# Optimization experiments

Hardware: AMD Instinct MI355X
Metric: run time of the kernel (lower is better)

## Reference

```python
import jax, jax.numpy as jnp
import numpy as np

B, T, IN, HID, HYP = 32, 1024, 512, 512, 256


def setup_inputs() -> dict:
    key = jax.random.key(0)
    ks = jax.random.split(key, 12)
    s = lambda *sh: 1.0 / np.sqrt(sh[-1])
    return {
        "x": jax.random.normal(ks[0], (B, T, IN), jnp.float32),
        "hidden": jax.random.normal(ks[1], (B, HID), jnp.float32),
        "W_start": jax.random.uniform(ks[2], (HYP, IN), jnp.float32, -s(HYP, IN), s(HYP, IN)),
        "b_start": jax.random.uniform(ks[3], (HYP,), jnp.float32, -s(HYP, IN), s(HYP, IN)),
        "W_mid": jax.random.uniform(ks[4], (HYP, HYP), jnp.float32, -s(HYP, HYP), s(HYP, HYP)),
        "b_mid": jax.random.uniform(ks[5], (HYP,), jnp.float32, -s(HYP, HYP), s(HYP, HYP)),
        "W_end": jax.random.uniform(ks[6], (HID, HYP), jnp.float32, -s(HID, HYP), s(HID, HYP)),
        "b_end": jax.random.uniform(ks[7], (HID,), jnp.float32, -s(HID, HYP), s(HID, HYP)),
        "W2": jax.random.uniform(ks[8], (HID, IN), jnp.float32, -s(HID, IN), s(HID, IN)),
        "b2": jax.random.uniform(ks[9], (HID,), jnp.float32, -s(HID, IN), s(HID, IN)),
    }


def _roll_sum_relu(b, hidden):
    # b: [B, T, H], hidden: [B, H]
    # recurrence: h_t = relu(roll(h_{t-1}, 1, axis=-1) + b_t)
    bt = jnp.swapaxes(b, 0, 1)  # [T, B, H]

    def step(h, b_t):
        h_new = jax.nn.relu(jnp.roll(h, 1, axis=-1) + b_t)
        return h_new, h_new

    _, outs = jax.lax.scan(step, hidden, bt)
    return jnp.swapaxes(outs, 0, 1)  # [B, T, H]


def reference(x, hidden, W_start, b_start, W_mid, b_mid, W_end, b_end, W2, b2):
    h = jax.nn.relu(jnp.einsum('bti,hi->bth', x, W_start) + b_start)
    h = jax.nn.relu(jnp.einsum('bth,gh->btg', h, W_mid) + b_mid)
    fc_end = jnp.einsum('btg,og->bto', h, W_end) + b_end
    sig = jax.nn.sigmoid(jnp.einsum('bti,oi->bto', x, W2) + b2)
    b = fc_end * sig  # [B, T, HID]
    outputs = _roll_sum_relu(b, hidden)
    return outputs, outputs[:, -1, :]
```

## Files before the change

### kernel.cpp

```cpp
#include <hip/hip_runtime.h>
#include <math.h>

#define B_   32
#define T_   1024
#define IN_  512
#define HID_ 512
#define HYP_ 256
#define M_   (B_ * T_)
#define R_   128
#define NSEG 8
#define SEGL 128
#define NCH  (B_ * HID_)

#define H1S  0
#define H2S  65536
#define STG  131072
#define LDS_BYTES 163840

typedef _Float16 half8_t __attribute__((ext_vector_type(8)));
typedef float    f32x4   __attribute__((ext_vector_type(4)));

typedef __attribute__((address_space(1))) const void* gptr_as1;
typedef __attribute__((address_space(3))) void*       lptr_as3;

__device__ __forceinline__ void gload_lds16(const void* g, void* l) {
    __builtin_amdgcn_global_load_lds((gptr_as1)g, (lptr_as3)l, 16, 0, 0);
}

#define VMCNT8() asm volatile("s_waitcnt vmcnt(8)" ::: "memory")
#define VMCNT4() asm volatile("s_waitcnt vmcnt(4)" ::: "memory")
#define VMCNT0() asm volatile("s_waitcnt vmcnt(0)" ::: "memory")
#define LGKM0()  asm volatile("s_waitcnt lgkmcnt(0)" ::: "memory")
#define SBAR()   __builtin_amdgcn_s_barrier()
#define SCHED0() __builtin_amdgcn_sched_barrier(0)

__global__ __launch_bounds__(256) void cvt_w(
    const float* __restrict__ Ws, _Float16* __restrict__ wsh,
    const float* __restrict__ Wm, _Float16* __restrict__ wmh,
    const float* __restrict__ We, _Float16* __restrict__ weh,
    const float* __restrict__ W2, _Float16* __restrict__ w2h)
{
    const int blk = blockIdx.x;
    const float* src; _Float16* dst; int base;
    if      (blk < 64)  { src = Ws; dst = wsh; base = blk; }
    else if (blk < 96)  { src = Wm; dst = wmh; base = blk - 64; }
    else if (blk < 160) { src = We; dst = weh; base = blk - 96; }
    else                { src = W2; dst = w2h; base = blk - 160; }
    const int i = base * 2048 + threadIdx.x * 8;
    f32x4 v0 = *(const f32x4*)(src + i);
    f32x4 v1 = *(const f32x4*)(src + i + 4);
    half8_t h;
    h[0] = (_Float16)v0[0]; h[1] = (_Float16)v0[1];
    h[2] = (_Float16)v0[2]; h[3] = (_Float16)v0[3];
    h[4] = (_Float16)v1[0]; h[5] = (_Float16)v1[1];
    h[6] = (_Float16)v1[2]; h[7] = (_Float16)v1[3];
    *(half8_t*)(dst + i) = h;
}

__device__ __forceinline__ void stage512(const _Float16* src, int K,
                                         char* ldsbase, int tid)
{
#pragma unroll
    for (int q = 0; q < 2; ++q) {
        const int s = q * 512 + tid;
        const int g = s >> 6, c2 = (s >> 4) & 3, r = (s & 15) ^ c2;
        const char* gp = (const char*)src + (size_t)(g * 16 + r) * (K * 2) + c2 * 16;
        char* lp = ldsbase + (q * 512 + (tid & ~63)) * 16;
        gload_lds16(gp, lp);
    }
}

__device__ __forceinline__ void stageW64(const _Float16* src, int K,
                                         char* ldsbase, int tid)
{
    stage512(src,      K, ldsbase,         tid);
    stage512(src + 32, K, ldsbase + 16384, tid);
}

__device__ __forceinline__ void ld_x32(const float* __restrict__ x, int m0,
                                       int ks, int tid, f32x4& a, f32x4& b)
{
    const int g = tid >> 6, c2 = (tid >> 4) & 3, r = (tid & 15) ^ c2;
    const float* p = x + (size_t)(m0 + g * 16 + r) * IN_ + ks + c2 * 8;
    a = *(const f32x4*)p;
    b = *(const f32x4*)(p + 4);
}

__device__ __forceinline__ void wr_x32(const f32x4& a, const f32x4& b,
                                       char* ldsbase, int tid)
{
    half8_t h;
    h[0] = (_Float16)a[0]; h[1] = (_Float16)a[1];
    h[2] = (_Float16)a[2]; h[3] = (_Float16)a[3];
    h[4] = (_Float16)b[0]; h[5] = (_Float16)b[1];
    h[6] = (_Float16)b[2]; h[7] = (_Float16)b[3];
    *(half8_t*)(ldsbase + tid * 16) = h;
}

__device__ __forceinline__ void do_step16(const char* ab, const char* bb,
                                          int wm, int wn, int lsw,
                                          f32x4 acc[4][4])
{
    half8_t af[4], wf[4];
#pragma unroll
    for (int i = 0; i < 4; ++i)
        af[i] = *(const half8_t*)(ab + (wm * 4 + i) * 1024 + lsw);
#pragma unroll
    for (int j = 0; j < 4; ++j)
        wf[j] = *(const half8_t*)(bb + (wn * 4 + j) * 1024 + lsw);
#pragma unroll
    for (int i = 0; i < 4; ++i)
#pragma unroll
        for (int j = 0; j < 4; ++j)
            acc[i][j] = __builtin_amdgcn_mfma_f32_16x16x32_f16(af[i], wf[j], acc[i][j], 0, 0, 0);
}

__device__ __forceinline__ void do_step32(const char* ab, const char* bb,
                                          int wm, int wn, int lsw,
                                          f32x4 acc[4][4])
{
    do_step16(ab,        bb,         wm, wn, lsw, acc);
    do_step16(ab + 8192, bb + 16384, wm, wn, lsw, acc);
}

__device__ __forceinline__ void epi_relu_lds(char* dst, const f32x4 acc[4][4],
                                             const float* __restrict__ bias,
                                             int wm, int wn, int lq, int lr)
{
#pragma unroll
    for (int j = 0; j < 4; ++j) {
        const int col = wn * 64 + j * 16 + lr;
        const float bv = bias[col];
        const int cc2 = (col & 31) >> 3;
        const int cpart = (col >> 5) * 8192 + cc2 * 256 + (col & 7) * 2;
#pragma unroll
        for (int i = 0; i < 4; ++i) {
#pragma unroll
            for (int rg = 0; rg < 4; ++rg) {
                const int row = wm * 64 + i * 16 + lq * 4 + rg;
                const float v = fmaxf(acc[i][j][rg] + bv, 0.f);
                *(_Float16*)(dst + cpart + (row >> 4) * 1024 +
                             (((row & 15) ^ cc2)) * 16) = (_Float16)v;
            }
        }
    }
}

__global__ __launch_bounds__(512, 2) void fused_mlp(
    const float* __restrict__ x,
    const _Float16* __restrict__ wsh, const float* __restrict__ bs,
    const _Float16* __restrict__ wmh, const float* __restrict__ bm,
    const _Float16* __restrict__ weh, const float* __restrict__ be,
    const _Float16* __restrict__ w2h, const float* __restrict__ b2,
    _Float16* __restrict__ bh)
{
    __shared__ __align__(16) char lds[LDS_BYTES];

    const int tid  = threadIdx.x;
    const int m0   = blockIdx.x * R_;
    const int lane = tid & 63;
    const int wave = tid >> 6;
    const int wm = wave >> 2;
    const int wn = wave & 3;
    const int lq = lane >> 4, lr = lane & 15;
    const int lsw = (lane ^ ((lane >> 4) & 3)) * 16;

    const f32x4 zero = {0.f, 0.f, 0.f, 0.f};

    {
        f32x4 acc[4][4];
#pragma unroll
        for (int i = 0; i < 4; ++i)
#pragma unroll
            for (int j = 0; j < 4; ++j) acc[i][j] = zero;

        {
            f32x4 pa0, pa1, pa2, pa3;
            ld_x32(x, m0, 0, tid, pa0, pa1);
            ld_x32(x, m0, 32, tid, pa2, pa3);
            stageW64(wsh, IN_, lds + STG, tid);
            wr_x32(pa0, pa1, lds + H2S, tid);
            wr_x32(pa2, pa3, lds + H2S + 8192, tid);
            __syncthreads();
        }
        for (int s = 0; s < 7; ++s) {
            const int e = s + 1;
            f32x4 pa0, pa1, pa2, pa3;
            ld_x32(x, m0, e * 64, tid, pa0, pa1);
            ld_x32(x, m0, e * 64 + 32, tid, pa2, pa3);
            SCHED0();
            stageW64(wsh + e * 64, IN_, (e & 1) ? lds + H2S + 32768 : lds + STG, tid);
            SCHED0(); VMCNT8(); SCHED0(); SBAR(); SCHED0();
            char* xb = lds + H2S + (e & 1) * 16384;
            wr_x32(pa0, pa1, xb, tid);
            wr_x32(pa2, pa3, xb + 8192, tid);
            const char* ab = lds + H2S + (s & 1) * 16384;
            const char* bb = (s & 1) ? lds + H2S + 32768 : lds + STG;
            __builtin_amdgcn_s_setprio(1);
            do_step32(ab, bb, wm, wn, lsw, acc);
            __builtin_amdgcn_s_setprio(0);
            LGKM0(); SCHED0(); SBAR(); SCHED0();
        }
        stageW64(wmh, HYP_, lds + STG, tid);
        SCHED0(); VMCNT4(); SCHED0(); SBAR(); SCHED0();
        __builtin_amdgcn_s_setprio(1);
        do_step32(lds + H2S + 16384, lds + H2S + 32768, wm, wn, lsw, acc);
        __builtin_amdgcn_s_setprio(0);
        __syncthreads();
        epi_relu_lds(lds + H1S, acc, bs, wm, wn, lq, lr);
        __syncthreads();
    }

    {
        f32x4 acc[4][4];
#pragma unroll
        for (int i = 0; i < 4; ++i)
#pragma unroll
            for (int j = 0; j < 4; ++j) acc[i][j] = zero;

        for (int s = 0; s < 3; ++s) {
            const int e = s + 1;
            stageW64(wmh + e * 64, HYP_, (e & 1) ? lds + H2S : lds + STG, tid);
            SCHED0(); VMCNT4(); SCHED0(); SBAR(); SCHED0();
            const char* ab = lds + H1S + s * 16384;
            const char* bb = (s & 1) ? lds + H2S : lds + STG;
            __builtin_amdgcn_s_setprio(1);
            do_step32(ab, bb, wm, wn, lsw, acc);
            __builtin_amdgcn_s_setprio(0);
            SCHED0(); SBAR(); SCHED0();
        }
        stageW64(weh, HYP_, lds + STG, tid);
        SCHED0(); VMCNT4(); SCHED0(); SBAR(); SCHED0();
        __builtin_amdgcn_s_setprio(1);
        do_step32(lds + H1S + 49152, lds + H2S, wm, wn, lsw, acc);
        __builtin_amdgcn_s_setprio(0);
        __syncthreads();
        epi_relu_lds(lds + H2S, acc, bm, wm, wn, lq, lr);
        __syncthreads();
    }

#pragma unroll 1
    for (int half = 0; half < 2; ++half) {
        const int c0 = half * 256;
        const _Float16* wehh = weh + (size_t)c0 * HYP_;
        const _Float16* w2hh = w2h + (size_t)c0 * IN_;
        f32x4 accf[4][4], accs[4][4];
#pragma unroll
        for (int i = 0; i < 4; ++i)
#pragma unroll
            for (int j = 0; j < 4; ++j) { accf[i][j] = zero; accs[i][j] = zero; }

        for (int s = 0; s < 3; ++s) {
            const int e = s + 1;
            stageW64(wehh + e * 64, HYP_, (e & 1) ? lds + H1S : lds + STG, tid);
            SCHED0(); VMCNT4(); SCHED0(); SBAR(); SCHED0();
            const char* ab = lds + H2S + s * 16384;
            const char* bb = (s & 1) ? lds + H1S : lds + STG;
            __builtin_amdgcn_s_setprio(1);
            do_step32(ab, bb, wm, wn, lsw, accf);
            __builtin_amdgcn_s_setprio(0);
            SCHED0(); SBAR(); SCHED0();
        }
        {
            f32x4 pa0, pa1, pa2, pa3;
            ld_x32(x, m0, 0, tid, pa0, pa1);
            ld_x32(x, m0, 32, tid, pa2, pa3);
            SCHED0();
            stageW64(w2hh, IN_, lds + STG, tid);
            SCHED0(); VMCNT8(); SCHED0(); SBAR(); SCHED0();
            wr_x32(pa0, pa1, lds + H1S + 32768, tid);
            wr_x32(pa2, pa3, lds + H1S + 32768 + 8192, tid);
            __builtin_amdgcn_s_setprio(1);
            do_step32(lds + H2S + 49152, lds + H1S, wm, wn, lsw, accf);
            __builtin_amdgcn_s_setprio(0);
            LGKM0(); SCHED0(); SBAR(); SCHED0();
        }
        for (int s = 0; s < 7; ++s) {
            const int e = s + 1;
            f32x4 pa0, pa1, pa2, pa3;
            ld_x32(x, m0, e * 64, tid, pa0, pa1);
            ld_x32(x, m0, e * 64 + 32, tid, pa2, pa3);
            SCHED0();
            stageW64(w2hh + e * 64, IN_, (e & 1) ? lds + H1S : lds + STG, tid);
            SCHED0(); VMCNT8(); SCHED0(); SBAR(); SCHED0();
            char* xb = lds + H1S + 32768 + (e & 1) * 16384;
            wr_x32(pa0, pa1, xb, tid);
            wr_x32(pa2, pa3, xb + 8192, tid);
            const char* ab = lds + H1S + 32768 + (s & 1) * 16384;
            const char* bb = (s & 1) ? lds + H1S : lds + STG;
            __builtin_amdgcn_s_setprio(1);
            do_step32(ab, bb, wm, wn, lsw, accs);
            __builtin_amdgcn_s_setprio(0);
            LGKM0(); SCHED0(); SBAR(); SCHED0();
        }
        if (half == 0) {
            stageW64(weh + (size_t)256 * HYP_, HYP_, lds + STG, tid);
            SCHED0(); VMCNT4();
        } else {
            VMCNT0();
        }
        SCHED0(); SBAR(); SCHED0();
        __builtin_amdgcn_s_setprio(1);
        do_step32(lds + H1S + 49152, lds + H1S, wm, wn, lsw, accs);
        __builtin_amdgcn_s_setprio(0);
        __syncthreads();

#pragma unroll
        for (int j = 0; j < 4; ++j) {
            const int gcol = c0 + wn * 64 + j * 16 + lr;
            const float bev = be[gcol];
            const float b2v = b2[gcol];
#pragma unroll
            for (int i = 0; i < 4; ++i) {
#pragma unroll
                for (int rg = 0; rg < 4; ++rg) {
                    const int row = m0 + wm * 64 + i * 16 + lq * 4 + rg;
                    const float fc = accf[i][j][rg] + bev;
                    float sg = accs[i][j][rg] + b2v;
                    sg = 1.f / (1.f + __expf(-sg));
                    bh[(size_t)row * HID_ + gcol] = (_Float16)(fc * sg);
                }
            }
        }
        __syncthreads();
    }
}

__global__ __launch_bounds__(256) void seg_reduce(const _Float16* __restrict__ bh,
                                                  float* __restrict__ Sarr,
                                                  float* __restrict__ Darr)
{
    const int G = blockIdx.x * 256 + threadIdx.x;
    const int r = G & 511;
    const int seg = (G >> 9) & 7;
    const int b = G >> 12;
    const int chain = b * 512 + r;
    const _Float16* bb = bh + (size_t)b * (T_ * HID_);
    const int t0 = seg * SEGL;

    float S = 0.f, D = -__builtin_inff();
#pragma unroll 8
    for (int u = 0; u < SEGL; ++u) {
        const int t = t0 + u;
        const float v = (float)bb[t * 512 + ((r + t) & 511)];
        S += v;
        D = fmaxf(D + v, 0.f);
    }
    Sarr[seg * NCH + chain] = S;
    Darr[seg * NCH + chain] = D;
}

__global__ __launch_bounds__(64) void carry_scan(const float* __restrict__ hidden,
                                                 const float* __restrict__ Sarr,
                                                 const float* __restrict__ Darr,
                                                 float* __restrict__ carry,
                                                 float* __restrict__ hlast)
{
    const int chain = blockIdx.x * 64 + threadIdx.x;
    const int b = chain >> 9, r = chain & 511;
    float c = hidden[b * 512 + ((r + 511) & 511)];
#pragma unroll
    for (int j = 0; j < NSEG; ++j) {
        carry[j * NCH + chain] = c;
        c = fmaxf(c + Sarr[j * NCH + chain], Darr[j * NCH + chain]);
    }
    hlast[b * 512 + ((r + 1023) & 511)] = c;
}

__global__ __launch_bounds__(256) void seg_apply(const _Float16* __restrict__ bh,
                                                 const float* __restrict__ carry,
                                                 float* __restrict__ out)
{
    const int G = blockIdx.x * 256 + threadIdx.x;
    const int r = G & 511;
    const int seg = (G >> 9) & 7;
    const int b = G >> 12;
    const int chain = b * 512 + r;
    const _Float16* bb = bh + (size_t)b * (T_ * HID_);
    float* ob = out + (size_t)b * (T_ * HID_);
    const int t0 = seg * SEGL;

    float c = carry[seg * NCH + chain];
#pragma unroll 8
    for (int u = 0; u < SEGL; ++u) {
        const int t = t0 + u;
        const int idx = t * 512 + ((r + t) & 511);
        c = fmaxf(c + (float)bb[idx], 0.f);
        ob[idx] = c;
    }
}

extern "C" void kernel_launch(void* const* d_in, const int* in_sizes, int n_in,
                              void* d_out, int out_size, void* d_ws, size_t ws_size,
                              hipStream_t stream)
{
    const float* x      = (const float*)d_in[0];
    const float* hidden = (const float*)d_in[1];
    const float* Ws     = (const float*)d_in[2];
    const float* bs     = (const float*)d_in[3];
    const float* Wm     = (const float*)d_in[4];
    const float* bm     = (const float*)d_in[5];
    const float* We     = (const float*)d_in[6];
    const float* be     = (const float*)d_in[7];
    const float* W2     = (const float*)d_in[8];
    const float* b2     = (const float*)d_in[9];

    float* outputs = (float*)d_out;
    float* hlast   = outputs + (size_t)M_ * HID_;

    _Float16* bh   = (_Float16*)d_ws;
    _Float16* wsh  = bh + (size_t)M_ * HID_;
    _Float16* wmh  = wsh + HYP_ * IN_;
    _Float16* weh  = wmh + HYP_ * HYP_;
    _Float16* w2h  = weh + HID_ * HYP_;
    float*    Sarr = (float*)(w2h + HID_ * IN_);
    float*    Darr = Sarr + NSEG * NCH;
    float*    carr = Darr + NSEG * NCH;

    cvt_w<<<dim3(288), 256, 0, stream>>>(Ws, wsh, Wm, wmh, We, weh, W2, w2h);
    fused_mlp<<<dim3(M_ / R_), 512, 0, stream>>>(
        x, wsh, bs, wmh, bm, weh, be, w2h, b2, bh);
    seg_reduce<<<dim3((NCH * NSEG) / 256), 256, 0, stream>>>(bh, Sarr, Darr);
    carry_scan<<<dim3(NCH / 64), 64, 0, stream>>>(hidden, Sarr, Darr, carr, hlast);
    seg_apply<<<dim3((NCH * NSEG) / 256), 256, 0, stream>>>(bh, carr, outputs);
}
```

Measured before the change: 126.9 us.

## Stage fp32 x tiles directly into LDS and convert to fp16 at fragment load

Replaces the register round-trip for x (global load to VGPRs, convert, then LDS write) with direct global-to-LDS async copies of the raw fp32 data. The fp16 conversion moves to the point where MFMA A fragments are read from LDS. The W2 phase is restructured into 16 smaller k-steps of 32 to fit the larger fp32 footprint. This removes the VGPR staging and the extra LDS writes and lgkm waits, in exchange for twice the LDS bytes per A tile, more LDS reads and conversions inside the MFMA loop, and more barriers in the W2 loop.

```diff
diff --git a/kernel.cpp b/kernel.cpp
--- a/kernel.cpp
+++ b/kernel.cpp
@@ -30,7 +30,6 @@
 #define VMCNT8() asm volatile("s_waitcnt vmcnt(8)" ::: "memory")
 #define VMCNT4() asm volatile("s_waitcnt vmcnt(4)" ::: "memory")
 #define VMCNT0() asm volatile("s_waitcnt vmcnt(0)" ::: "memory")
-#define LGKM0()  asm volatile("s_waitcnt lgkmcnt(0)" ::: "memory")
 #define SBAR()   __builtin_amdgcn_s_barrier()
 #define SCHED0() __builtin_amdgcn_sched_barrier(0)
 
@@ -77,24 +76,33 @@
     stage512(src + 32, K, ldsbase + 16384, tid);
 }
 
-__device__ __forceinline__ void ld_x32(const float* __restrict__ x, int m0,
-                                       int ks, int tid, f32x4& a, f32x4& b)
-{
-    const int g = tid >> 6, c2 = (tid >> 4) & 3, r = (tid & 15) ^ c2;
-    const float* p = x + (size_t)(m0 + g * 16 + r) * IN_ + ks + c2 * 8;
-    a = *(const f32x4*)p;
-    b = *(const f32x4*)(p + 4);
-}
-
-__device__ __forceinline__ void wr_x32(const f32x4& a, const f32x4& b,
-                                       char* ldsbase, int tid)
+__device__ __forceinline__ void stageA32(const float* src, int K,
+                                         char* ldsbase, int tid)
+{
+#pragma unroll
+    for (int p = 0; p < 2; ++p) {
+        const int g = tid >> 6, c2 = (tid >> 4) & 3, r = (tid & 15) ^ c2;
+        const char* gp = (const char*)(src + (size_t)(g * 16 + r) * K + c2 * 8 + p * 4);
+        char* lp = ldsbase + p * 8192 + (tid & ~63) * 16;
+        gload_lds16(gp, lp);
+    }
+}
+
+__device__ __forceinline__ void stageA32_64(const float* src, int K,
+                                            char* ldsbase, int tid)
+{
+    stageA32(src,      K, ldsbase,         tid);
+    stageA32(src + 32, K, ldsbase + 16384, tid);
+}
+
+__device__ __forceinline__ half8_t cvt8(f32x4 a, f32x4 b)
 {
     half8_t h;
     h[0] = (_Float16)a[0]; h[1] = (_Float16)a[1];
     h[2] = (_Float16)a[2]; h[3] = (_Float16)a[3];
     h[4] = (_Float16)b[0]; h[5] = (_Float16)b[1];
     h[6] = (_Float16)b[2]; h[7] = (_Float16)b[3];
-    *(half8_t*)(ldsbase + tid * 16) = h;
+    return h;
 }
 
 __device__ __forceinline__ void do_step16(const char* ab, const char* bb,
@@ -119,8 +127,37 @@
                                           int wm, int wn, int lsw,
                                           f32x4 acc[4][4])
 {
-    do_step16(ab,        bb,         wm, wn, lsw, acc);
-    do_step16(ab + 8192, bb + 16384, wm, wn, lsw, acc);
+    do_step16(ab,         bb,         wm, wn, lsw, acc);
+    do_step16(ab + 8192,  bb + 16384, wm, wn, lsw, acc);
+}
+
+__device__ __forceinline__ void do_step16_fa(const char* ab, const char* bb,
+                                             int wm, int wn, int lsw,
+                                             f32x4 acc[4][4])
+{
+    half8_t af[4], wf[4];
+#pragma unroll
+    for (int i = 0; i < 4; ++i) {
+        f32x4 p0 = *(const f32x4*)(ab + (wm * 4 + i) * 1024 + lsw);
+        f32x4 p1 = *(const f32x4*)(ab + 8192 + (wm * 4 + i) * 1024 + lsw);
+        af[i] = cvt8(p0, p1);
+    }
+#pragma unroll
+    for (int j = 0; j < 4; ++j)
+        wf[j] = *(const half8_t*)(bb + (wn * 4 + j) * 1024 + lsw);
+#pragma unroll
+    for (int i = 0; i < 4; ++i)
+#pragma unroll
+        for (int j = 0; j < 4; ++j)
+            acc[i][j] = __builtin_amdgcn_mfma_f32_16x16x32_f16(af[i], wf[j], acc[i][j], 0, 0, 0);
+}
+
+__device__ __forceinline__ void do_step32_fa(const char* ab, const char* bb,
+                                             int wm, int wn, int lsw,
+                                             f32x4 acc[4][4])
+{
+    do_step16_fa(ab,          bb,         wm, wn, lsw, acc);
+    do_step16_fa(ab + 16384,  bb + 16384, wm, wn, lsw, acc);
 }
 
 __device__ __forceinline__ void epi_relu_lds(char* dst, const f32x4 acc[4][4],
@@ -165,6 +202,7 @@
     const int lq = lane >> 4, lr = lane & 15;
     const int lsw = (lane ^ ((lane >> 4) & 3)) * 16;
 
+    const float* xrow = x + (size_t)m0 * IN_;
     const f32x4 zero = {0.f, 0.f, 0.f, 0.f};
 
     {
@@ -174,37 +212,26 @@
 #pragma unroll
             for (int j = 0; j < 4; ++j) acc[i][j] = zero;
 
-        {
-            f32x4 pa0, pa1, pa2, pa3;
-            ld_x32(x, m0, 0, tid, pa0, pa1);
-            ld_x32(x, m0, 32, tid, pa2, pa3);
-            stageW64(wsh, IN_, lds + STG, tid);
-            wr_x32(pa0, pa1, lds + H2S, tid);
-            wr_x32(pa2, pa3, lds + H2S + 8192, tid);
-            __syncthreads();
-        }
+        stageA32_64(xrow, IN_, lds + H2S, tid);
+        stageW64(wsh, IN_, lds + STG, tid);
+        __syncthreads();
+
         for (int s = 0; s < 7; ++s) {
             const int e = s + 1;
-            f32x4 pa0, pa1, pa2, pa3;
-            ld_x32(x, m0, e * 64, tid, pa0, pa1);
-            ld_x32(x, m0, e * 64 + 32, tid, pa2, pa3);
-            SCHED0();
-            stageW64(wsh + e * 64, IN_, (e & 1) ? lds + H2S + 32768 : lds + STG, tid);
+            stageA32_64(xrow + e * 64, IN_, lds + H2S + (e & 1) * 32768, tid);
+            stageW64(wsh + e * 64, IN_, (e & 1) ? lds + H1S : lds + STG, tid);
             SCHED0(); VMCNT8(); SCHED0(); SBAR(); SCHED0();
-            char* xb = lds + H2S + (e & 1) * 16384;
-            wr_x32(pa0, pa1, xb, tid);
-            wr_x32(pa2, pa3, xb + 8192, tid);
-            const char* ab = lds + H2S + (s & 1) * 16384;
-            const char* bb = (s & 1) ? lds + H2S + 32768 : lds + STG;
+            const char* ab = lds + H2S + (s & 1) * 32768;
+            const char* bb = (s & 1) ? lds + H1S : lds + STG;
             __builtin_amdgcn_s_setprio(1);
-            do_step32(ab, bb, wm, wn, lsw, acc);
+            do_step32_fa(ab, bb, wm, wn, lsw, acc);
             __builtin_amdgcn_s_setprio(0);
-            LGKM0(); SCHED0(); SBAR(); SCHED0();
+            SCHED0(); SBAR(); SCHED0();
         }
         stageW64(wmh, HYP_, lds + STG, tid);
         SCHED0(); VMCNT4(); SCHED0(); SBAR(); SCHED0();
         __builtin_amdgcn_s_setprio(1);
-        do_step32(lds + H2S + 16384, lds + H2S + 32768, wm, wn, lsw, acc);
+        do_step32_fa(lds + H2S + 32768, lds + H1S, wm, wn, lsw, acc);
         __builtin_amdgcn_s_setprio(0);
         __syncthreads();
         epi_relu_lds(lds + H1S, acc, bs, wm, wn, lq, lr);
@@ -262,36 +289,25 @@
             SCHED0(); SBAR(); SCHED0();
         }
         {
-            f32x4 pa0, pa1, pa2, pa3;
-            ld_x32(x, m0, 0, tid, pa0, pa1);
-            ld_x32(x, m0, 32, tid, pa2, pa3);
-            SCHED0();
-            stageW64(w2hh, IN_, lds + STG, tid);
-            SCHED0(); VMCNT8(); SCHED0(); SBAR(); SCHED0();
-            wr_x32(pa0, pa1, lds + H1S + 32768, tid);
-            wr_x32(pa2, pa3, lds + H1S + 32768 + 8192, tid);
+            stageA32(xrow, IN_, lds + H1S + 32768, tid);
+            stage512(w2hh, IN_, lds + STG, tid);
+            SCHED0(); VMCNT4(); SCHED0(); SBAR(); SCHED0();
             __builtin_amdgcn_s_setprio(1);
             do_step32(lds + H2S + 49152, lds + H1S, wm, wn, lsw, accf);
             __builtin_amdgcn_s_setprio(0);
-            LGKM0(); SCHED0(); SBAR(); SCHED0();
-        }
-        for (int s = 0; s < 7; ++s) {
+            SCHED0(); SBAR(); SCHED0();
+        }
+        for (int s = 0; s < 15; ++s) {
             const int e = s + 1;
-            f32x4 pa0, pa1, pa2, pa3;
-            ld_x32(x, m0, e * 64, tid, pa0, pa1);
-            ld_x32(x, m0, e * 64 + 32, tid, pa2, pa3);
-            SCHED0();
-            stageW64(w2hh + e * 64, IN_, (e & 1) ? lds + H1S : lds + STG, tid);
-            SCHED0(); VMCNT8(); SCHED0(); SBAR(); SCHED0();
-            char* xb = lds + H1S + 32768 + (e & 1) * 16384;
-            wr_x32(pa0, pa1, xb, tid);
-            wr_x32(pa2, pa3, xb + 8192, tid);
+            stageA32(xrow + e * 32, IN_, lds + H1S + 32768 + (e & 1) * 16384, tid);
+            stage512(w2hh + e * 32, IN_, (e & 1) ? lds + H1S : lds + STG, tid);
+            SCHED0(); VMCNT4(); SCHED0(); SBAR(); SCHED0();
             const char* ab = lds + H1S + 32768 + (s & 1) * 16384;
             const char* bb = (s & 1) ? lds + H1S : lds + STG;
             __builtin_amdgcn_s_setprio(1);
-            do_step32(ab, bb, wm, wn, lsw, accs);
+            do_step16_fa(ab, bb, wm, wn, lsw, accs);
             __builtin_amdgcn_s_setprio(0);
-            LGKM0(); SCHED0(); SBAR(); SCHED0();
+            SCHED0(); SBAR(); SCHED0();
         }
         if (half == 0) {
             stageW64(weh + (size_t)256 * HYP_, HYP_, lds + STG, tid);
@@ -301,7 +317,7 @@
         }
         SCHED0(); SBAR(); SCHED0();
         __builtin_amdgcn_s_setprio(1);
-        do_step32(lds + H1S + 49152, lds + H1S, wm, wn, lsw, accs);
+        do_step16_fa(lds + H1S + 32768 + 16384, lds + H1S, wm, wn, lsw, accs);
         __builtin_amdgcn_s_setprio(0);
         __syncthreads();
 
```

Result: faster. 112.9 us (-11.0%).
